# Optimization experiments

Hardware: AMD Instinct MI355X
Metric: run time of the kernel (lower is better)

The kernel has to match this reference:

```python
import jax, jax.numpy as jnp
import numpy as np

T = 1024
B = 64
A = 128
ABSTRACT_PENALTY = 0.5
CONSISTENCY_RATIO = 1.0
NEG = -1e30  # acts as log(0) mask; exp underflows to exactly 0 in logsumexp
STOP_IX, CONT_IX = 0, 1


def setup_inputs() -> dict:
    key = jax.random.key(0)
    k1, k2, k3, k4, k5 = jax.random.split(key, 5)
    actions = jax.random.randint(k1, (T,), 0, A, dtype=jnp.int32)
    action_logps = jax.nn.log_softmax(jax.random.normal(k2, (T + 1, B, A), dtype=jnp.float32), axis=-1)
    stop_logps = jax.nn.log_softmax(jax.random.normal(k3, (T + 1, B, 2), dtype=jnp.float32), axis=-1)
    start_logps = jax.nn.log_softmax(jax.random.normal(k4, (T + 1, B), dtype=jnp.float32), axis=-1)
    consistency_penalties = -0.1 * jnp.abs(jax.random.normal(k5, (T + 1, T + 1, B), dtype=jnp.float32))
    return {
        'actions': actions,
        'action_logps': action_logps,
        'stop_logps': stop_logps,
        'start_logps': start_logps,
        'consistency_penalties': consistency_penalties,
    }


def _hsmm_loss(actions, action_logps, stop_logps, start_logps, consistency_penalties):
    T_ = actions.shape[0]
    b = start_logps.shape[1]
    # option_step_dist as fixed (T, b) buffer, rows > current step masked to NEG
    dist0 = jnp.full((T_, b), NEG, dtype=action_logps.dtype).at[0].set(start_logps[0])
    # step i=0: only the action logp (no stop/start rearrange, no consistency pen)
    logp0 = jax.nn.logsumexp(dist0 + action_logps[0, :, actions[0]][None, :])

    idx = jnp.arange(1, T_)
    stop_lps = stop_logps[1:T_, :, STOP_IX]          # (T-1, b)
    cont_lps = stop_logps[1:T_, :, CONT_IX]          # (T-1, b)
    start_lps = start_logps[1:T_]                    # (T-1, b)
    act_lps = action_logps[idx, :, actions[1:]]      # (T-1, b)
    # column i of consistency_penalties, rows :T (masked dist rows kill rows > i)
    cons_cols = jnp.transpose(consistency_penalties[:T_, 1:T_, :], (1, 0, 2))  # (T-1, T, b)

    def step(carry, xs):
        dist, logp, cons = carry
        i, stop_lp, cont_lp, start_lp, act_lp, cp = xs
        total_rearrange = jax.nn.logsumexp(dist + stop_lp[None, :]) - ABSTRACT_PENALTY
        new_mass = start_lp + total_rearrange
        dist = (dist + cont_lp[None, :]).at[i].set(new_mass)
        cons = cons + jax.nn.logsumexp(dist + cp)
        logp = logp + jax.nn.logsumexp(dist + act_lp[None, :])
        return (dist, logp, cons), None

    init = (dist0, logp0, jnp.zeros((), dist0.dtype))
    (dist, logp, cons), _ = jax.lax.scan(step, init, (idx, stop_lps, cont_lps, start_lps, act_lps, cons_cols))
    total_logp = logp + jax.nn.logsumexp(dist + stop_logps[T_, :, STOP_IX][None, :])
    return -total_logp + CONSISTENCY_RATIO * cons


def reference(actions, action_logps, stop_logps, start_logps, consistency_penalties):
    return _hsmm_loss(actions, action_logps, stop_logps, start_logps, consistency_penalties)
```

## Files before the change

kernel.cpp:

```cpp
#include <hip/hip_runtime.h>

#define T_N 1024
#define B_N 64
#define A_N 128
#define TP1 1025

typedef float f32x4 __attribute__((ext_vector_type(4)));

__device__ __forceinline__ float bcf(int x){ return __builtin_bit_cast(float, x); }
__device__ __forceinline__ int   bci(float x){ return __builtin_bit_cast(int, x); }

template<int CTRL, int RM>
__device__ __forceinline__ float dpp_add_step(float x){
  int t = __builtin_amdgcn_update_dpp(0, bci(x), CTRL, RM, 0xf, true);
  return x + bcf(t);
}
__device__ __forceinline__ float wave_sum64(float x){
  x = dpp_add_step<0x111,0xf>(x);
  x = dpp_add_step<0x112,0xf>(x);
  x = dpp_add_step<0x114,0xf>(x);
  x = dpp_add_step<0x118,0xf>(x);
  x = dpp_add_step<0x142,0xa>(x);
  x = dpp_add_step<0x143,0xc>(x);
  return bcf(__builtin_amdgcn_readlane(bci(x), 63));
}
__device__ __forceinline__ void wave_sum64_x4(float a, float b, float c, float d,
                                              float& ra, float& rb, float& rc, float& rd){
  a = dpp_add_step<0x111,0xf>(a); b = dpp_add_step<0x111,0xf>(b);
  c = dpp_add_step<0x111,0xf>(c); d = dpp_add_step<0x111,0xf>(d);
  a = dpp_add_step<0x112,0xf>(a); b = dpp_add_step<0x112,0xf>(b);
  c = dpp_add_step<0x112,0xf>(c); d = dpp_add_step<0x112,0xf>(d);
  a = dpp_add_step<0x114,0xf>(a); b = dpp_add_step<0x114,0xf>(b);
  c = dpp_add_step<0x114,0xf>(c); d = dpp_add_step<0x114,0xf>(d);
  a = dpp_add_step<0x118,0xf>(a); b = dpp_add_step<0x118,0xf>(b);
  c = dpp_add_step<0x118,0xf>(c); d = dpp_add_step<0x118,0xf>(d);
  a = dpp_add_step<0x142,0xa>(a); b = dpp_add_step<0x142,0xa>(b);
  c = dpp_add_step<0x142,0xa>(c); d = dpp_add_step<0x142,0xa>(d);
  a = dpp_add_step<0x143,0xc>(a); b = dpp_add_step<0x143,0xc>(b);
  c = dpp_add_step<0x143,0xc>(c); d = dpp_add_step<0x143,0xc>(d);
  ra = bcf(__builtin_amdgcn_readlane(bci(a), 63));
  rb = bcf(__builtin_amdgcn_readlane(bci(b), 63));
  rc = bcf(__builtin_amdgcn_readlane(bci(c), 63));
  rd = bcf(__builtin_amdgcn_readlane(bci(d), 63));
}
__device__ __forceinline__ float group16_sum(float x){
  x = dpp_add_step<0x111,0xf>(x);
  x = dpp_add_step<0x112,0xf>(x);
  x = dpp_add_step<0x114,0xf>(x);
  x = dpp_add_step<0x118,0xf>(x);
  return x;
}
template<int CTRL, int RM>
__device__ __forceinline__ float dpp_max_step(float x){
  int t = __builtin_amdgcn_update_dpp(bci(-3.4e38f), bci(x), CTRL, RM, 0xf, false);
  return fmaxf(x, bcf(t));
}
__device__ __forceinline__ float wave_max64(float x){
  x = dpp_max_step<0x111,0xf>(x);
  x = dpp_max_step<0x112,0xf>(x);
  x = dpp_max_step<0x114,0xf>(x);
  x = dpp_max_step<0x118,0xf>(x);
  x = dpp_max_step<0x142,0xa>(x);
  x = dpp_max_step<0x143,0xc>(x);
  return bcf(__builtin_amdgcn_readlane(bci(x), 63));
}

__global__ __launch_bounds__(256) void prep_kernel(
    const float* __restrict__ stop_logps,
    const float* __restrict__ start_logps,
    float* __restrict__ quadQ,
    float* __restrict__ cs,
    float* __restrict__ A1p)
{
  const int tid  = (int)threadIdx.x;
  const int lane = tid & 63;
  const int wv   = tid >> 6;
  const int p    = (int)blockIdx.x * 4 + wv;
  const float KAPPA = 0.60653065971263342f;
  const float2* stop2 = (const float2*)stop_logps;

  int g = (int)blockIdx.x * 256 + tid;
  A1p[g] = 0.f; A1p[g + 16384] = 0.f; A1p[g + 32768] = 0.f; A1p[g + 49152] = 0.f;

  if (p < 255) {
    const int i1 = 4 * p + 1;
    float2 q1 = stop2[(i1 + 0) * B_N + lane];
    float2 q2 = stop2[(i1 + 1) * B_N + lane];
    float2 q3 = stop2[(i1 + 2) * B_N + lane];
    float2 q4 = stop2[(i1 + 3) * B_N + lane];
    float t1 = start_logps[(i1 + 0) * B_N + lane];
    float t2 = start_logps[(i1 + 1) * B_N + lane];
    float t3 = start_logps[(i1 + 2) * B_N + lane];
    float t4 = start_logps[(i1 + 3) * B_N + lane];
    float e1 = __expf(q1.x), c1 = __expf(q1.y), s1 = KAPPA * __expf(t1);
    float e2 = __expf(q2.x), c2 = __expf(q2.y), s2 = KAPPA * __expf(t2);
    float e3 = __expf(q3.x), c3 = __expf(q3.y), s3 = KAPPA * __expf(t3);
    float e4 = __expf(q4.x), c4 = __expf(q4.y), s4 = KAPPA * __expf(t4);

    float V1 = e1;
    float V2 = e2 * c1;
    float V3 = e3 * c2 * c1;
    float V4 = e4 * c3 * c2 * c1;

    float k21 = wave_sum64(e2 * s1);
    float k31 = wave_sum64(e3 * c2 * s1);
    float k32 = wave_sum64(e3 * s2);
    float k41 = wave_sum64(e4 * c3 * c2 * s1);
    float k42 = wave_sum64(e4 * c3 * s2);
    float k43 = wave_sum64(e4 * s3);

    f32x4* qs = (f32x4*)quadQ;
    size_t base = (size_t)p * 5 * 64 + lane;
    qs[base + 0 * 64] = (f32x4){V1, V2, V3, V4};
    qs[base + 1 * 64] = (f32x4){c1, s1, c2, s2};
    qs[base + 2 * 64] = (f32x4){c3, s3, c4, s4};
    qs[base + 3 * 64] = (f32x4){k21, k31, k32, k41};
    qs[base + 4 * 64] = (f32x4){k42, k43, 0.f, 0.f};
  }

  if (blockIdx.x < 16 && wv == 0) {
    int c = (int)blockIdx.x;
    float s = 0.f;
    for (int k = 1; k <= 64; ++k) {
      int i = 64 * c + k;
      if (i <= 1023) s += stop2[i * B_N + lane].y;
    }
    cs[c * B_N + lane] = s;
  }
}

__global__ __launch_bounds__(64, 1) void scan_kernel(
    const float* __restrict__ stop_logps,
    const float* __restrict__ start_logps,
    const float* __restrict__ quadQ,
    float* __restrict__ z_ws,
    float* __restrict__ r_ws,
    float* __restrict__ wexp)
{
  const int lane = threadIdx.x;
  const float2* stop2 = (const float2*)stop_logps;

  float2 sct0 = stop2[1021 * B_N + lane];
  float2 sct1 = stop2[1022 * B_N + lane];
  float2 sct2 = stop2[1023 * B_N + lane];
  float stt0 = start_logps[1021 * B_N + lane];
  float stt1 = start_logps[1022 * B_N + lane];
  float stt2 = start_logps[1023 * B_N + lane];

  float z = __expf(start_logps[lane]);

  const f32x4* qs = (const f32x4*)quadQ;

  f32x4 qb[8][5];
  #pragma unroll
  for (int q = 0; q < 8; ++q)
    #pragma unroll
    for (int s = 0; s < 5; ++s)
      qb[q][s] = qs[((size_t)q * 5 + s) * 64 + lane];

  for (int p0 = 0; p0 < 248; p0 += 8) {
    #pragma unroll
    for (int q = 0; q < 8; ++q) {
      const int p  = p0 + q;
      const int i1 = 4 * p + 1;
      f32x4 V   = qb[q][0];
      f32x4 C12 = qb[q][1];
      f32x4 C34 = qb[q][2];
      f32x4 K1  = qb[q][3];
      f32x4 K2  = qb[q][4];
      {
        const int pn = p + 8;
        #pragma unroll
        for (int s = 0; s < 5; ++s)
          qb[q][s] = qs[((size_t)pn * 5 + s) * 64 + lane];
      }

      float d1, d2, d3, d4;
      wave_sum64_x4(z * V.x, z * V.y, z * V.z, z * V.w, d1, d2, d3, d4);
      float r1 = d1;
      float r2 = __builtin_fmaf(K1.x, r1, d2);
      float r3 = __builtin_fmaf(K1.z, r2, __builtin_fmaf(K1.y, r1, d3));
      float r4 = __builtin_fmaf(K2.y, r3,
                 __builtin_fmaf(K2.x, r2, __builtin_fmaf(K1.w, r1, d4)));

      float z1 = __builtin_fmaf(r1, C12.y, z  * C12.x);
      float z2 = __builtin_fmaf(r2, C12.w, z1 * C12.z);
      float z3 = __builtin_fmaf(r3, C34.y, z2 * C34.x);
      float z4 = __builtin_fmaf(r4, C34.w, z3 * C34.z);
      z_ws[(i1 + 0) * B_N + lane] = z1;
      z_ws[(i1 + 1) * B_N + lane] = z2;
      z_ws[(i1 + 2) * B_N + lane] = z3;
      z_ws[(i1 + 3) * B_N + lane] = z4;
      if (lane == 0) *(f32x4*)(r_ws + 4 * p) = (f32x4){r1, r2, r3, r4};
      z = z4;

      if ((q & 3) == 3) {
        int rb  = bci(r4);
        int e16 = ((rb >> 23) & 255) - 127;
        z = ldexpf(z, -e16);
        if (lane == 0) wexp[p >> 2] = (float)e16;
      }
    }
  }
  #pragma unroll
  for (int q = 0; q < 7; ++q) {
    const int p  = 248 + q;
    const int i1 = 4 * p + 1;
    f32x4 V   = qb[q][0];
    f32x4 C12 = qb[q][1];
    f32x4 C34 = qb[q][2];
    f32x4 K1  = qb[q][3];
    f32x4 K2  = qb[q][4];
    float d1, d2, d3, d4;
    wave_sum64_x4(z * V.x, z * V.y, z * V.z, z * V.w, d1, d2, d3, d4);
    float r1 = d1;
    float r2 = __builtin_fmaf(K1.x, r1, d2);
    float r3 = __builtin_fmaf(K1.z, r2, __builtin_fmaf(K1.y, r1, d3));
    float r4 = __builtin_fmaf(K2.y, r3,
               __builtin_fmaf(K2.x, r2, __builtin_fmaf(K1.w, r1, d4)));
    float z1 = __builtin_fmaf(r1, C12.y, z  * C12.x);
    float z2 = __builtin_fmaf(r2, C12.w, z1 * C12.z);
    float z3 = __builtin_fmaf(r3, C34.y, z2 * C34.x);
    float z4 = __builtin_fmaf(r4, C34.w, z3 * C34.z);
    z_ws[(i1 + 0) * B_N + lane] = z1;
    z_ws[(i1 + 1) * B_N + lane] = z2;
    z_ws[(i1 + 2) * B_N + lane] = z3;
    z_ws[(i1 + 3) * B_N + lane] = z4;
    if (lane == 0) *(f32x4*)(r_ws + 4 * p) = (f32x4){r1, r2, r3, r4};
    z = z4;
    if (q == 3) {
      int rb  = bci(r4);
      int e16 = ((rb >> 23) & 255) - 127;
      z = ldexpf(z, -e16);
      if (lane == 0) wexp[62] = (float)e16;
    }
  }
  const float KAPPA = 0.60653065971263342f;
  {
    float esw = __expf(sct0.x), ecw = __expf(sct0.y), sv = KAPPA * __expf(stt0);
    float r = wave_sum64(z * esw);
    z = __builtin_fmaf(sv, r, z * ecw);
    z_ws[1021 * B_N + lane] = z;
    if (lane == 0) r_ws[1020] = r;
  }
  {
    float esw = __expf(sct1.x), ecw = __expf(sct1.y), sv = KAPPA * __expf(stt1);
    float r = wave_sum64(z * esw);
    z = __builtin_fmaf(sv, r, z * ecw);
    z_ws[1022 * B_N + lane] = z;
    if (lane == 0) r_ws[1021] = r;
  }
  {
    float esw = __expf(sct2.x), ecw = __expf(sct2.y), sv = KAPPA * __expf(stt2);
    float r = wave_sum64(z * esw);
    z = __builtin_fmaf(sv, r, z * ecw);
    z_ws[1023 * B_N + lane] = z;
    if (lane == 0) r_ws[1022] = r;
  }
}

__global__ __launch_bounds__(1024) void post_kernel(
    const int* __restrict__ actions,
    const float* __restrict__ action_logps,
    const float* __restrict__ stop_logps,
    const float* __restrict__ start_logps,
    const float* __restrict__ z_ws,
    const float* __restrict__ r_ws,
    const float* __restrict__ wexp,
    const float* __restrict__ cs,
    float* __restrict__ u_ws,
    float* __restrict__ D_ws,
    float* __restrict__ out)
{
  const int tid  = (int)threadIdx.x;
  const int w    = tid >> 6;
  const int lane = tid & 63;
  const float LN2 = 0.69314718055994531f;
  const float2* stop2 = (const float2*)stop_logps;

  __shared__ float Pw[64];
  if (w == 0) {
    float psum = 0.f;
    for (int m = 0; m < lane && m < 63; ++m) psum += wexp[m];
    Pw[lane] = psum * LN2;
  }
  __syncthreads();

  float C = 0.f;
  for (int ww = 0; ww < w; ++ww) C += cs[ww * B_N + lane];
  for (int k = 1; k <= 64; ++k) {
    int i = 64 * w + k;
    if (i > 1023) break;
    C += stop2[i * B_N + lane].y;
    float Pv = Pw[(i - 1) >> 4];
    float R  = __logf(r_ws[i - 1]) + Pv - 0.5f;
    u_ws[i * B_N + lane] = start_logps[i * B_N + lane] + R - C;
    float zs = wave_sum64(z_ws[i * B_N + lane]);
    D_ws[i * B_N + lane] = C - (__logf(zs) + Pv);
  }
  if (tid < 64) u_ws[lane] = start_logps[lane];

  if (w == 15) {
    float st0 = start_logps[lane];
    int   a0  = actions[0];
    float al0 = action_logps[lane * A_N + a0];
    float lp0 = __logf(wave_sum64(__expf(st0 + al0)));
    float stopT = stop_logps[(T_N * B_N + lane) * 2 + 0];
    float z1023 = z_ws[1023 * B_N + lane];
    float fin = __logf(wave_sum64(z1023 * __expf(stopT))) + Pw[63];
    if (lane == 0) out[0] = -(lp0 + fin);
  }
}

__global__ __launch_bounds__(256) void cons_logp_kernel(
    const float* __restrict__ cons_pen,
    const float* __restrict__ u_ws,
    const float* __restrict__ D_ws,
    const int* __restrict__ actions,
    const float* __restrict__ action_logps,
    float* __restrict__ A1p,
    float* __restrict__ LQ)
{
  const int bid  = (int)blockIdx.x;
  const int tid  = (int)threadIdx.x;
  const int lane = tid & 63;
  const int wv   = tid >> 6;

  __shared__ float sm[4][64];
  __shared__ float sa[4][64];

  if (bid < 512) {
    const int bq  = (lane & 15) * 4;
    const int row = lane >> 4;
    #pragma unroll
    for (int t = 0; t < 2; ++t) {
      const int j = t ? (1023 - bid) : bid;
      const float4 u4 = *(const float4*)(u_ws + j * B_N + bq);
      float* dst = A1p + ((j & 63) << 10);
      for (int i0 = j + 4 * wv; i0 <= 1023; i0 += 16) {
        int i  = i0 + row;
        int iL = i > 1023 ? 1023 : i;
        f32x4 cp4 = __builtin_nontemporal_load(
            (const f32x4*)(cons_pen + ((size_t)j * TP1 + iL) * B_N + bq));
        float4 d4  = *(const float4*)(D_ws + (size_t)iL * B_N + bq);
        bool valid = (i >= 1) && (i <= 1023);
        float a0 = u4.x + d4.x + cp4.x;
        float a1 = u4.y + d4.y + cp4.y;
        float a2 = u4.z + d4.z + cp4.z;
        float a3 = u4.w + d4.w + cp4.w;
        a0 = valid ? a0 : -1e30f;
        a1 = valid ? a1 : -1e30f;
        a2 = valid ? a2 : -1e30f;
        a3 = valid ? a3 : -1e30f;
        float sred = (__expf(a0) + __expf(a1)) + (__expf(a2) + __expf(a3));
        sred = group16_sum(sred);
        if (((lane & 15) == 15) && valid) atomicAdd(dst + i, sred);
      }
    }
  } else {
    const int i = 1535 - bid;
    int   ai = actions[i];
    float av = action_logps[((size_t)i * B_N + lane) * A_N + ai];

    float mA = -1e30f, aA = 0.f, mB = -1e30f, aB = 0.f;
    for (int jj = wv; jj <= i; jj += 8) {
      float u0 = u_ws[jj * B_N + lane];
      int   j1 = jj + 4;
      float u1 = (j1 <= i) ? u_ws[j1 * B_N + lane] : -1e30f;
      float n0 = fmaxf(mA, u0);
      aA = aA * __expf(mA - n0) + __expf(u0 - n0);
      mA = n0;
      float n1 = fmaxf(mB, u1);
      aB = aB * __expf(mB - n1) + __expf(u1 - n1);
      mB = n1;
    }
    float m   = fmaxf(mA, mB);
    float acc = aA * __expf(mA - m) + aB * __expf(mB - m);

    sm[wv][lane] = m; sa[wv][lane] = acc;
    __syncthreads();
    if (wv == 0) {
      float m0 = sm[0][lane], m1 = sm[1][lane], m2 = sm[2][lane], m3 = sm[3][lane];
      float M2 = fmaxf(fmaxf(m0, m1), fmaxf(m2, m3));
      float A  = sa[0][lane] * __expf(m0 - M2) + sa[1][lane] * __expf(m1 - M2)
               + sa[2][lane] * __expf(m2 - M2) + sa[3][lane] * __expf(m3 - M2);
      float S  = M2 + __logf(A);
      float val = S + D_ws[(size_t)i * B_N + lane] + av;
      float mx  = wave_max64(val);
      float sum = wave_sum64(__expf(val - mx));
      if (lane == 0) LQ[i] = mx + __logf(sum);
    }
  }
}

__global__ __launch_bounds__(256) void finish_kernel(
    const float* __restrict__ A1p,
    const float* __restrict__ LQ,
    float* __restrict__ out)
{
  const int i = (int)blockIdx.x * 256 + (int)threadIdx.x;
  float v = 0.f;
  if (i >= 1 && i <= 1023) {
    float a = 0.f;
    #pragma unroll 8
    for (int p = 0; p < 64; ++p) a += A1p[(p << 10) + i];
    v = __logf(a) - LQ[i];
  }
  float ws = wave_sum64(v);
  __shared__ float sb[4];
  if ((threadIdx.x & 63) == 0) sb[threadIdx.x >> 6] = ws;
  __syncthreads();
  if (threadIdx.x == 0) atomicAdd(out, sb[0] + sb[1] + sb[2] + sb[3]);
}

extern "C" void kernel_launch(void* const* d_in, const int* in_sizes, int n_in,
                              void* d_out, int out_size, void* d_ws, size_t ws_size,
                              hipStream_t stream) {
  const int*   actions      = (const int*)d_in[0];
  const float* action_logps = (const float*)d_in[1];
  const float* stop_logps   = (const float*)d_in[2];
  const float* start_logps  = (const float*)d_in[3];
  const float* cons_pen     = (const float*)d_in[4];
  float* out = (float*)d_out;

  float* z_ws  = (float*)d_ws;
  float* u_ws  = z_ws + T_N * B_N;
  float* D_ws  = u_ws + T_N * B_N;
  float* A1p   = D_ws + T_N * B_N;
  float* r_ws  = A1p + 64 * 1024;
  float* wexp  = r_ws + T_N;
  float* LQ    = wexp + 64;
  float* cs    = LQ + T_N;
  float* quadQ = cs + 16 * B_N;

  hipLaunchKernelGGL(prep_kernel, dim3(64), dim3(256), 0, stream,
                     stop_logps, start_logps, quadQ, cs, A1p);
  hipLaunchKernelGGL(scan_kernel, dim3(1), dim3(64), 0, stream,
                     stop_logps, start_logps, quadQ, z_ws, r_ws, wexp);
  hipLaunchKernelGGL(post_kernel, dim3(1), dim3(1024), 0, stream,
                     actions, action_logps, stop_logps, start_logps,
                     z_ws, r_ws, wexp, cs, u_ws, D_ws, out);
  hipLaunchKernelGGL(cons_logp_kernel, dim3(1535), dim3(256), 0, stream,
                     cons_pen, u_ws, D_ws, actions, action_logps, A1p, LQ);
  hipLaunchKernelGGL(finish_kernel, dim3(4), dim3(256), 0, stream,
                     A1p, LQ, out);
}
```

Measured before the change: 489.7 us.

## Collapse scan's per-quad z update and recompute intermediate z in post kernel

```diff
diff --git a/kernel.cpp b/kernel.cpp
--- a/kernel.cpp
+++ b/kernel.cpp
@@ -97,10 +97,18 @@
     float e3 = __expf(q3.x), c3 = __expf(q3.y), s3 = KAPPA * __expf(t3);
     float e4 = __expf(q4.x), c4 = __expf(q4.y), s4 = KAPPA * __expf(t4);
 
+    float c21  = c2 * c1;
+    float c321 = c3 * c21;
     float V1 = e1;
     float V2 = e2 * c1;
-    float V3 = e3 * c2 * c1;
-    float V4 = e4 * c3 * c2 * c1;
+    float V3 = e3 * c21;
+    float V4 = e4 * c321;
+
+    float Cq = c4 * c321;
+    float S1 = c4 * c3 * c2 * s1;
+    float S2 = c4 * c3 * s2;
+    float S3 = c4 * s3;
+    float S4 = s4;
 
     float k21 = wave_sum64(e2 * s1);
     float k31 = wave_sum64(e3 * c2 * s1);
@@ -110,12 +118,11 @@
     float k43 = wave_sum64(e4 * s3);
 
     f32x4* qs = (f32x4*)quadQ;
-    size_t base = (size_t)p * 5 * 64 + lane;
+    size_t base = (size_t)p * 4 * 64 + lane;
     qs[base + 0 * 64] = (f32x4){V1, V2, V3, V4};
-    qs[base + 1 * 64] = (f32x4){c1, s1, c2, s2};
-    qs[base + 2 * 64] = (f32x4){c3, s3, c4, s4};
-    qs[base + 3 * 64] = (f32x4){k21, k31, k32, k41};
-    qs[base + 4 * 64] = (f32x4){k42, k43, 0.f, 0.f};
+    qs[base + 1 * 64] = (f32x4){Cq, S1, S2, S3};
+    qs[base + 2 * 64] = (f32x4){S4, k21, k31, k32};
+    qs[base + 3 * 64] = (f32x4){k41, k42, k43, 0.f};
   }
 
   if (blockIdx.x < 16 && wv == 0) {
@@ -151,49 +158,45 @@
 
   const f32x4* qs = (const f32x4*)quadQ;
 
-  f32x4 qb[8][5];
+  f32x4 qb[8][4];
   #pragma unroll
   for (int q = 0; q < 8; ++q)
     #pragma unroll
-    for (int s = 0; s < 5; ++s)
-      qb[q][s] = qs[((size_t)q * 5 + s) * 64 + lane];
+    for (int s = 0; s < 4; ++s)
+      qb[q][s] = qs[((size_t)q * 4 + s) * 64 + lane];
 
   for (int p0 = 0; p0 < 248; p0 += 8) {
     #pragma unroll
     for (int q = 0; q < 8; ++q) {
-      const int p  = p0 + q;
-      const int i1 = 4 * p + 1;
-      f32x4 V   = qb[q][0];
-      f32x4 C12 = qb[q][1];
-      f32x4 C34 = qb[q][2];
-      f32x4 K1  = qb[q][3];
-      f32x4 K2  = qb[q][4];
+      const int p = p0 + q;
+      f32x4 V = qb[q][0];
+      f32x4 Z = qb[q][1];
+      f32x4 W = qb[q][2];
+      f32x4 X = qb[q][3];
       {
         const int pn = p + 8;
         #pragma unroll
-        for (int s = 0; s < 5; ++s)
-          qb[q][s] = qs[((size_t)pn * 5 + s) * 64 + lane];
+        for (int s = 0; s < 4; ++s)
+          qb[q][s] = qs[((size_t)pn * 4 + s) * 64 + lane];
       }
 
       float d1, d2, d3, d4;
       wave_sum64_x4(z * V.x, z * V.y, z * V.z, z * V.w, d1, d2, d3, d4);
       float r1 = d1;
-      float r2 = __builtin_fmaf(K1.x, r1, d2);
-      float r3 = __builtin_fmaf(K1.z, r2, __builtin_fmaf(K1.y, r1, d3));
-      float r4 = __builtin_fmaf(K2.y, r3,
-                 __builtin_fmaf(K2.x, r2, __builtin_fmaf(K1.w, r1, d4)));
-
-      float z1 = __builtin_fmaf(r1, C12.y, z  * C12.x);
-      float z2 = __builtin_fmaf(r2, C12.w, z1 * C12.z);
-      float z3 = __builtin_fmaf(r3, C34.y, z2 * C34.x);
-      float z4 = __builtin_fmaf(r4, C34.w, z3 * C34.z);
-      z_ws[(i1 + 0) * B_N + lane] = z1;
-      z_ws[(i1 + 1) * B_N + lane] = z2;
-      z_ws[(i1 + 2) * B_N + lane] = z3;
-      z_ws[(i1 + 3) * B_N + lane] = z4;
+      float r2 = __builtin_fmaf(W.y, r1, d2);
+      float r3 = __builtin_fmaf(W.w, r2, __builtin_fmaf(W.z, r1, d3));
+      float r4 = __builtin_fmaf(X.z, r3,
+                 __builtin_fmaf(X.y, r2, __builtin_fmaf(X.x, r1, d4)));
       if (lane == 0) *(f32x4*)(r_ws + 4 * p) = (f32x4){r1, r2, r3, r4};
-      z = z4;
-
+
+      z = __builtin_fmaf(r4, W.x,
+          __builtin_fmaf(r3, Z.w,
+          __builtin_fmaf(r2, Z.z,
+          __builtin_fmaf(r1, Z.y, z * Z.x))));
+
+      if (q == 7 && (p0 & 8)) {
+        z_ws[(4 * p + 4) * B_N + lane] = z;
+      }
       if ((q & 3) == 3) {
         int rb  = bci(r4);
         int e16 = ((rb >> 23) & 255) - 127;
@@ -204,30 +207,22 @@
   }
   #pragma unroll
   for (int q = 0; q < 7; ++q) {
-    const int p  = 248 + q;
-    const int i1 = 4 * p + 1;
-    f32x4 V   = qb[q][0];
-    f32x4 C12 = qb[q][1];
-    f32x4 C34 = qb[q][2];
-    f32x4 K1  = qb[q][3];
-    f32x4 K2  = qb[q][4];
+    f32x4 V = qb[q][0];
+    f32x4 Z = qb[q][1];
+    f32x4 W = qb[q][2];
+    f32x4 X = qb[q][3];
     float d1, d2, d3, d4;
     wave_sum64_x4(z * V.x, z * V.y, z * V.z, z * V.w, d1, d2, d3, d4);
     float r1 = d1;
-    float r2 = __builtin_fmaf(K1.x, r1, d2);
-    float r3 = __builtin_fmaf(K1.z, r2, __builtin_fmaf(K1.y, r1, d3));
-    float r4 = __builtin_fmaf(K2.y, r3,
-               __builtin_fmaf(K2.x, r2, __builtin_fmaf(K1.w, r1, d4)));
-    float z1 = __builtin_fmaf(r1, C12.y, z  * C12.x);
-    float z2 = __builtin_fmaf(r2, C12.w, z1 * C12.z);
-    float z3 = __builtin_fmaf(r3, C34.y, z2 * C34.x);
-    float z4 = __builtin_fmaf(r4, C34.w, z3 * C34.z);
-    z_ws[(i1 + 0) * B_N + lane] = z1;
-    z_ws[(i1 + 1) * B_N + lane] = z2;
-    z_ws[(i1 + 2) * B_N + lane] = z3;
-    z_ws[(i1 + 3) * B_N + lane] = z4;
-    if (lane == 0) *(f32x4*)(r_ws + 4 * p) = (f32x4){r1, r2, r3, r4};
-    z = z4;
+    float r2 = __builtin_fmaf(W.y, r1, d2);
+    float r3 = __builtin_fmaf(W.w, r2, __builtin_fmaf(W.z, r1, d3));
+    float r4 = __builtin_fmaf(X.z, r3,
+               __builtin_fmaf(X.y, r2, __builtin_fmaf(X.x, r1, d4)));
+    if (lane == 0) *(f32x4*)(r_ws + 4 * (248 + q)) = (f32x4){r1, r2, r3, r4};
+    z = __builtin_fmaf(r4, W.x,
+        __builtin_fmaf(r3, Z.w,
+        __builtin_fmaf(r2, Z.z,
+        __builtin_fmaf(r1, Z.y, z * Z.x))));
     if (q == 3) {
       int rb  = bci(r4);
       int e16 = ((rb >> 23) & 255) - 127;
@@ -240,26 +235,23 @@
     float esw = __expf(sct0.x), ecw = __expf(sct0.y), sv = KAPPA * __expf(stt0);
     float r = wave_sum64(z * esw);
     z = __builtin_fmaf(sv, r, z * ecw);
-    z_ws[1021 * B_N + lane] = z;
     if (lane == 0) r_ws[1020] = r;
   }
   {
     float esw = __expf(sct1.x), ecw = __expf(sct1.y), sv = KAPPA * __expf(stt1);
     float r = wave_sum64(z * esw);
     z = __builtin_fmaf(sv, r, z * ecw);
-    z_ws[1022 * B_N + lane] = z;
     if (lane == 0) r_ws[1021] = r;
   }
   {
     float esw = __expf(sct2.x), ecw = __expf(sct2.y), sv = KAPPA * __expf(stt2);
     float r = wave_sum64(z * esw);
     z = __builtin_fmaf(sv, r, z * ecw);
-    z_ws[1023 * B_N + lane] = z;
     if (lane == 0) r_ws[1022] = r;
   }
 }
 
-__global__ __launch_bounds__(1024) void post_kernel(
+__global__ __launch_bounds__(64) void post_kernel(
     const int* __restrict__ actions,
     const float* __restrict__ action_logps,
     const float* __restrict__ stop_logps,
@@ -272,33 +264,49 @@
     float* __restrict__ D_ws,
     float* __restrict__ out)
 {
-  const int tid  = (int)threadIdx.x;
-  const int w    = tid >> 6;
-  const int lane = tid & 63;
-  const float LN2 = 0.69314718055994531f;
+  const int w    = (int)blockIdx.x;
+  const int lane = (int)threadIdx.x;
+  const float LN2   = 0.69314718055994531f;
+  const float KAPPA = 0.60653065971263342f;
   const float2* stop2 = (const float2*)stop_logps;
 
-  __shared__ float Pw[64];
-  if (w == 0) {
-    float psum = 0.f;
-    for (int m = 0; m < lane && m < 63; ++m) psum += wexp[m];
-    Pw[lane] = psum * LN2;
-  }
-  __syncthreads();
+  float wl = (lane < 63) ? wexp[lane] : 0.f;
+
+  float Pv = LN2 * wave_sum64((lane < 4 * w) ? wl : 0.f);
+  float e0 = bcf(__builtin_amdgcn_readlane(bci(wl), 4 * w + 0));
+  float e1 = bcf(__builtin_amdgcn_readlane(bci(wl), 4 * w + 1));
+  float e2 = bcf(__builtin_amdgcn_readlane(bci(wl), 4 * w + 2));
 
   float C = 0.f;
   for (int ww = 0; ww < w; ++ww) C += cs[ww * B_N + lane];
+
+  float z;
+  if (w == 0) {
+    z = __expf(start_logps[lane]);
+    u_ws[lane] = start_logps[lane];
+  } else {
+    float em = bcf(__builtin_amdgcn_readlane(bci(wl), 4 * w - 1));
+    z = ldexpf(z_ws[(64 * w) * B_N + lane], -(int)em);
+  }
+
   for (int k = 1; k <= 64; ++k) {
     int i = 64 * w + k;
     if (i > 1023) break;
-    C += stop2[i * B_N + lane].y;
-    float Pv = Pw[(i - 1) >> 4];
-    float R  = __logf(r_ws[i - 1]) + Pv - 0.5f;
-    u_ws[i * B_N + lane] = start_logps[i * B_N + lane] + R - C;
-    float zs = wave_sum64(z_ws[i * B_N + lane]);
+    float cont = stop2[i * B_N + lane].y;
+    float stv  = start_logps[i * B_N + lane];
+    float r    = r_ws[i - 1];
+    C += cont;
+    float ecw = __expf(cont);
+    float sv  = KAPPA * __expf(stv);
+    z = __builtin_fmaf(r, sv, ecw * z);
+    float zs = wave_sum64(z);
+    float R  = __logf(r) + Pv - 0.5f;
+    u_ws[i * B_N + lane] = stv + R - C;
     D_ws[i * B_N + lane] = C - (__logf(zs) + Pv);
-  }
-  if (tid < 64) u_ws[lane] = start_logps[lane];
+    if (k == 16)      { z = ldexpf(z, -(int)e0); Pv += LN2 * e0; }
+    else if (k == 32) { z = ldexpf(z, -(int)e1); Pv += LN2 * e1; }
+    else if (k == 48) { z = ldexpf(z, -(int)e2); Pv += LN2 * e2; }
+  }
 
   if (w == 15) {
     float st0 = start_logps[lane];
@@ -306,8 +314,7 @@
     float al0 = action_logps[lane * A_N + a0];
     float lp0 = __logf(wave_sum64(__expf(st0 + al0)));
     float stopT = stop_logps[(T_N * B_N + lane) * 2 + 0];
-    float z1023 = z_ws[1023 * B_N + lane];
-    float fin = __logf(wave_sum64(z1023 * __expf(stopT))) + Pw[63];
+    float fin = __logf(wave_sum64(z * __expf(stopT))) + Pv;
     if (lane == 0) out[0] = -(lp0 + fin);
   }
 }
@@ -437,7 +444,7 @@
                      stop_logps, start_logps, quadQ, cs, A1p);
   hipLaunchKernelGGL(scan_kernel, dim3(1), dim3(64), 0, stream,
                      stop_logps, start_logps, quadQ, z_ws, r_ws, wexp);
-  hipLaunchKernelGGL(post_kernel, dim3(1), dim3(1024), 0, stream,
+  hipLaunchKernelGGL(post_kernel, dim3(16), dim3(64), 0, stream,
                      actions, action_logps, stop_logps, start_logps,
                      z_ws, r_ws, wexp, cs, u_ws, D_ws, out);
   hipLaunchKernelGGL(cons_logp_kernel, dim3(1535), dim3(256), 0, stream,
```

After: 481.1 us. No clear change (-1.8%).
